# Kernel optimization log

Measured on AMD Instinct MI355X. Metric: run time of the kernel, lower is better.

Reference implementation:

```python
import jax, jax.numpy as jnp
import numpy as np

B, N, E = 4096, 64, 256      # graph pairs, nodes per drug, directed edges per drug
F, H, FP = 128, 64, 2048     # node feat dim, hidden dim, fingerprint dim


def setup_inputs() -> dict:
    key = jax.random.key(0)
    ks = jax.random.split(key, 14)
    return {
        "x1": jax.random.normal(ks[0], (B, N, F), jnp.float32),
        "x2": jax.random.normal(ks[1], (B, N, F), jnp.float32),
        "edge1": jax.random.randint(ks[2], (B, 2, E), 0, N, jnp.int32),
        "edge2": jax.random.randint(ks[3], (B, 2, E), 0, N, jnp.int32),
        "fp1": jax.random.uniform(ks[4], (B, FP), jnp.float32),
        "fp2": jax.random.uniform(ks[5], (B, FP), jnp.float32),
        "W1": jax.random.normal(ks[6], (F, H), jnp.float32) * 0.05,
        "b1": jnp.zeros((H,), jnp.float32),
        "W2": jax.random.normal(ks[7], (H, H), jnp.float32) * 0.05,
        "b2": jnp.zeros((H,), jnp.float32),
        "Wm1": jax.random.normal(ks[8], (2 * H + 2 * FP, 256), jnp.float32) * 0.02,
        "bm1": jnp.zeros((256,), jnp.float32),
        "Wm2": jax.random.normal(ks[9], (256, 1), jnp.float32) * 0.05,
        "bm2": jnp.zeros((1,), jnp.float32),
    }


def gcn_conv(x, src, dst, W, b):
    """PyG GCNConv: self-loops + symmetric normalization, aggregated at dst."""
    n = x.shape[0]
    loops = jnp.arange(n, dtype=src.dtype)
    s = jnp.concatenate([src, loops])
    d = jnp.concatenate([dst, loops])
    deg = jax.ops.segment_sum(jnp.ones_like(d, jnp.float32), d, num_segments=n)
    norm = jax.lax.rsqrt(deg)                      # deg >= 1 due to self-loops
    xw = x @ W                                     # [n, H]
    msg = xw[s] * (norm[s] * norm[d])[:, None]     # [n+E, H]
    return jax.ops.segment_sum(msg, d, num_segments=n) + b


def encode(x, edges, W1, b1, W2, b2):
    src, dst = edges[0], edges[1]
    h = jax.nn.relu(gcn_conv(x, src, dst, W1, b1))
    h = jax.nn.relu(gcn_conv(h, src, dst, W2, b2))
    return h.mean(axis=0)                          # global_mean_pool (1 graph)


_encode_b = jax.vmap(encode, in_axes=(0, 0, None, None, None, None))


def reference(x1, x2, edge1, edge2, fp1, fp2, W1, b1, W2, b2, Wm1, bm1, Wm2, bm2):
    h1 = _encode_b(x1, edge1, W1, b1, W2, b2)      # [B, H]
    h2 = _encode_b(x2, edge2, W1, b1, W2, b2)      # [B, H]
    fused = jnp.concatenate([h1, h2, fp1, fp2], axis=1)  # [B, 2H+2FP]
    hidden = jax.nn.relu(fused @ Wm1 + bm1)
    return jax.nn.sigmoid(hidden @ Wm2 + bm2).reshape(-1)
```

## Files before the change

kernel.cpp:

```cpp
#include <hip/hip_runtime.h>
#include <math.h>

#define B_PAIRS 4096
#define NNODES  64
#define NEDGES  256
#define FDIM    128
#define HDIM    64
#define FPDIM   2048
#define MDIM    256
#define KTOT    4224

typedef __attribute__((ext_vector_type(4))) float f32x4;
typedef __bf16 bf16x8 __attribute__((ext_vector_type(8)));

__device__ __forceinline__ unsigned short f2bf(float f) {
    return __builtin_bit_cast(unsigned short, (__bf16)f);
}
__device__ __forceinline__ unsigned pack2(float a, float b) {
    return (unsigned)f2bf(a) | ((unsigned)f2bf(b) << 16);
}
__device__ __forceinline__ unsigned long long pack4(float a, float b, float c, float d) {
    return (unsigned long long)pack2(a, b) | ((unsigned long long)pack2(c, d) << 32);
}

__global__ void prep_weights(const float* __restrict__ W1, const float* __restrict__ W2,
                             unsigned short* __restrict__ W1t, unsigned short* __restrict__ W2t) {
    const int t0 = blockIdx.x * 256 + threadIdx.x;
    const int stride = gridDim.x * 256;
    for (int i = t0; i < HDIM * FDIM; i += stride) {
        const int n = i >> 7, k = i & 127;
        W1t[i] = f2bf(W1[k * HDIM + n]);
    }
    for (int i = t0; i < HDIM * HDIM; i += stride) {
        const int n = i >> 6, k = i & 63;
        W2t[i] = f2bf(W2[k * HDIM + n]);
    }
}

__global__ __launch_bounds__(256)
void prep_wm1(const float* __restrict__ Wm1, unsigned short* __restrict__ Wm1t) {
    __shared__ float tile[32][33];
    const int k0 = blockIdx.x * 32, n0 = blockIdx.y * 32;
    const int t = threadIdx.x;
    const int c = t & 31, r8 = t >> 5;
    #pragma unroll
    for (int rr = r8; rr < 32; rr += 8)
        tile[rr][c] = Wm1[(size_t)(k0 + rr) * MDIM + n0 + c];
    __syncthreads();
    #pragma unroll
    for (int j = 0; j < 4; ++j) {
        const int n = n0 + r8 + 8 * j;
        Wm1t[(size_t)n * KTOT + k0 + c] = f2bf(tile[c][r8 + 8 * j]);
    }
}

#define WAITLDS() do { __asm__ volatile("s_waitcnt lgkmcnt(0)" ::: "memory"); \
                       __builtin_amdgcn_sched_barrier(0); } while (0)

__global__ __launch_bounds__(64, 2)
void encode_kernel(const float* __restrict__ x1, const float* __restrict__ x2,
                   const int* __restrict__ e1, const int* __restrict__ e2,
                   const unsigned short* __restrict__ W1t, const float* __restrict__ b1,
                   const unsigned short* __restrict__ W2t, const float* __restrict__ b2,
                   float* __restrict__ hbuf) {
    __shared__ __align__(16) unsigned char lds[24576];
    const int gid  = blockIdx.x;
    const int drug = gid >> 12;
    const int b    = gid & (B_PAIRS - 1);
    const float* x  = (drug ? x2 : x1) + (size_t)b * NNODES * FDIM;
    const int*   eg = (drug ? e2 : e1) + (size_t)b * 2 * NEDGES;

    const int t  = threadIdx.x;
    const int lr = t & 15, lg = t >> 4;
    const unsigned swl = (unsigned)(lr & 7) << 4;

    unsigned* cnt = (unsigned*)(lds + 8192);
    int*      deg = (int*)(lds + 16640);
    float*    nrm = (float*)(lds + 16896);

    float4 xa[32];
    #pragma unroll
    for (int mt = 0; mt < 4; ++mt) {
        const float* xr = x + (size_t)(16 * mt + lr) * FDIM + 8 * lg;
        #pragma unroll
        for (int ks = 0; ks < 4; ++ks) {
            xa[mt * 8 + 2 * ks]     = ((const float4*)(xr + 32 * ks))[0];
            xa[mt * 8 + 2 * ks + 1] = ((const float4*)(xr + 32 * ks))[1];
        }
    }
    const int4 s4 = ((const int4*)eg)[t];
    const int4 d4 = ((const int4*)eg)[t + 64];

    #pragma unroll
    for (int i = 0; i < 8; ++i) ((uint4*)cnt)[t + 64 * i] = make_uint4(0, 0, 0, 0);
    if (t < 16) ((uint4*)cnt)[512 + t] = make_uint4(0, 0, 0, 0);
    deg[t] = 0;
    WAITLDS();

    {
        const int ss[4] = {s4.x, s4.y, s4.z, s4.w};
        const int dd[4] = {d4.x, d4.y, d4.z, d4.w};
        #pragma unroll
        for (int i = 0; i < 4; ++i) {
            atomicAdd(&deg[dd[i]], 1);
            atomicAdd(&cnt[dd[i] * 33 + (ss[i] >> 1)], 1u << ((ss[i] & 1) * 16));
        }
    }
    WAITLDS();
    nrm[t] = rsqrtf((float)deg[t] + 1.0f);
    WAITLDS();

    bf16x8 bw1[16];
    #pragma unroll
    for (int nt = 0; nt < 4; ++nt)
        #pragma unroll
        for (int ks = 0; ks < 4; ++ks)
            bw1[nt * 4 + ks] = *(const bf16x8*)(W1t + (16 * nt + lr) * FDIM + 32 * ks + 8 * lg);

    {
        const int r = t;
        const float nr = nrm[r];
        unsigned char* arow = lds + r * 128;
        const unsigned sw = (unsigned)(r & 7) << 4;
        #pragma unroll
        for (int cw = 0; cw < 16; ++cw) {
            const unsigned w0 = cnt[r * 33 + 2 * cw];
            const unsigned w1 = cnt[r * 33 + 2 * cw + 1];
            const float4 nv = ((const float4*)nrm)[cw];
            const int c = 4 * cw;
            const float u0 = (float)((w0 & 0xffffu) + (r == c     ? 1u : 0u)) * nr * nv.x;
            const float u1 = (float)((w0 >> 16)     + (r == c + 1 ? 1u : 0u)) * nr * nv.y;
            const float u2 = (float)((w1 & 0xffffu) + (r == c + 2 ? 1u : 0u)) * nr * nv.z;
            const float u3 = (float)((w1 >> 16)     + (r == c + 3 ? 1u : 0u)) * nr * nv.w;
            *(unsigned long long*)(arow + (((unsigned)(8 * cw)) ^ sw)) = pack4(u0, u1, u2, u3);
        }
    }
    WAITLDS();

    #pragma unroll
    for (int mt = 0; mt < 4; ++mt) {
        f32x4 acc[4];
        #pragma unroll
        for (int nt = 0; nt < 4; ++nt) acc[nt] = (f32x4){0.f, 0.f, 0.f, 0.f};
        #pragma unroll
        for (int ks = 0; ks < 4; ++ks) {
            bf16x8 a;
            const float4 u = xa[mt * 8 + 2 * ks], v = xa[mt * 8 + 2 * ks + 1];
            a[0] = (__bf16)u.x; a[1] = (__bf16)u.y; a[2] = (__bf16)u.z; a[3] = (__bf16)u.w;
            a[4] = (__bf16)v.x; a[5] = (__bf16)v.y; a[6] = (__bf16)v.z; a[7] = (__bf16)v.w;
            #pragma unroll
            for (int nt = 0; nt < 4; ++nt)
                acc[nt] = __builtin_amdgcn_mfma_f32_16x16x32_bf16(a, bw1[nt * 4 + ks], acc[nt], 0, 0, 0);
        }
        const unsigned m2 = (unsigned)(2 * (16 * mt + 4 * lg));
        #pragma unroll
        for (int nt = 0; nt < 4; ++nt) {
            const int f = 16 * nt + lr;
            *(unsigned long long*)(lds + 8192u + (unsigned)f * 128 + (m2 ^ swl)) =
                pack4(acc[nt][0], acc[nt][1], acc[nt][2], acc[nt][3]);
        }
    }
    WAITLDS();

    {
        bf16x8 ba[8];
        #pragma unroll
        for (int nt = 0; nt < 4; ++nt)
            #pragma unroll
            for (int ks = 0; ks < 2; ++ks)
                ba[nt * 2 + ks] = *(const bf16x8*)(lds + (unsigned)(16 * nt + lr) * 128 +
                                                   (((unsigned)(64 * ks + 16 * lg)) ^ swl));
        #pragma unroll
        for (int mt = 0; mt < 4; ++mt) {
            f32x4 acc[4];
            #pragma unroll
            for (int nt = 0; nt < 4; ++nt) acc[nt] = (f32x4){0.f, 0.f, 0.f, 0.f};
            #pragma unroll
            for (int ks = 0; ks < 2; ++ks) {
                const bf16x8 a = *(const bf16x8*)(lds + 8192u + (unsigned)(16 * mt + lr) * 128 +
                                                  (((unsigned)(64 * ks + 16 * lg)) ^ swl));
                #pragma unroll
                for (int nt = 0; nt < 4; ++nt)
                    acc[nt] = __builtin_amdgcn_mfma_f32_16x16x32_bf16(a, ba[nt * 2 + ks], acc[nt], 0, 0, 0);
            }
            const int m0 = 16 * mt + 4 * lg;
            const float4 b1v = *(const float4*)(b1 + m0);
            const unsigned m2 = (unsigned)(2 * m0);
            #pragma unroll
            for (int nt = 0; nt < 4; ++nt) {
                const int d = 16 * nt + lr;
                const float v0 = fmaxf(acc[nt][0] + b1v.x, 0.f);
                const float v1 = fmaxf(acc[nt][1] + b1v.y, 0.f);
                const float v2 = fmaxf(acc[nt][2] + b1v.z, 0.f);
                const float v3 = fmaxf(acc[nt][3] + b1v.w, 0.f);
                *(unsigned long long*)(lds + 16384u + (unsigned)d * 128 + (m2 ^ swl)) =
                    pack4(v0, v1, v2, v3);
            }
        }
    }
    WAITLDS();

    {
        bf16x8 bw2[8];
        #pragma unroll
        for (int nt = 0; nt < 4; ++nt)
            #pragma unroll
            for (int ks = 0; ks < 2; ++ks)
                bw2[nt * 2 + ks] = *(const bf16x8*)(W2t + (16 * nt + lr) * HDIM + 32 * ks + 8 * lg);
        #pragma unroll
        for (int mt = 0; mt < 4; ++mt) {
            f32x4 acc[4];
            #pragma unroll
            for (int nt = 0; nt < 4; ++nt) acc[nt] = (f32x4){0.f, 0.f, 0.f, 0.f};
            #pragma unroll
            for (int ks = 0; ks < 2; ++ks) {
                const bf16x8 a = *(const bf16x8*)(lds + 16384u + (unsigned)(16 * mt + lr) * 128 +
                                                  (((unsigned)(64 * ks + 16 * lg)) ^ swl));
                #pragma unroll
                for (int nt = 0; nt < 4; ++nt)
                    acc[nt] = __builtin_amdgcn_mfma_f32_16x16x32_bf16(a, bw2[nt * 2 + ks], acc[nt], 0, 0, 0);
            }
            const unsigned m2 = (unsigned)(2 * (16 * mt + 4 * lg));
            #pragma unroll
            for (int nt = 0; nt < 4; ++nt) {
                const int n = 16 * nt + lr;
                *(unsigned long long*)(lds + 8192u + (unsigned)n * 128 + (m2 ^ swl)) =
                    pack4(acc[nt][0], acc[nt][1], acc[nt][2], acc[nt][3]);
            }
        }
    }
    WAITLDS();

    {
        bf16x8 bt3[8];
        #pragma unroll
        for (int nt = 0; nt < 4; ++nt)
            #pragma unroll
            for (int ks = 0; ks < 2; ++ks)
                bt3[nt * 2 + ks] = *(const bf16x8*)(lds + 8192u + (unsigned)(16 * nt + lr) * 128 +
                                                    (((unsigned)(64 * ks + 16 * lg)) ^ swl));
        float b2v[4], p[4];
        #pragma unroll
        for (int nt = 0; nt < 4; ++nt) { b2v[nt] = b2[16 * nt + lr]; p[nt] = 0.f; }
        #pragma unroll
        for (int mt = 0; mt < 4; ++mt) {
            f32x4 acc[4];
            #pragma unroll
            for (int nt = 0; nt < 4; ++nt) acc[nt] = (f32x4){0.f, 0.f, 0.f, 0.f};
            #pragma unroll
            for (int ks = 0; ks < 2; ++ks) {
                const bf16x8 a = *(const bf16x8*)(lds + (unsigned)(16 * mt + lr) * 128 +
                                                  (((unsigned)(64 * ks + 16 * lg)) ^ swl));
                #pragma unroll
                for (int nt = 0; nt < 4; ++nt)
                    acc[nt] = __builtin_amdgcn_mfma_f32_16x16x32_bf16(a, bt3[nt * 2 + ks], acc[nt], 0, 0, 0);
            }
            #pragma unroll
            for (int nt = 0; nt < 4; ++nt) {
                #pragma unroll
                for (int j = 0; j < 4; ++j) p[nt] += fmaxf(acc[nt][j] + b2v[nt], 0.f);
            }
        }
        #pragma unroll
        for (int nt = 0; nt < 4; ++nt) {
            p[nt] += __shfl_xor(p[nt], 16, 64);
            p[nt] += __shfl_xor(p[nt], 32, 64);
        }
        if (lg == 0) {
            float* hout = hbuf + ((size_t)drug * B_PAIRS + b) * HDIM;
            #pragma unroll
            for (int nt = 0; nt < 4; ++nt) hout[16 * nt + lr] = p[nt] * (1.0f / 64.0f);
        }
    }
}

__global__ __launch_bounds__(256)
void fused_mlp_kernel(const float* __restrict__ fp1, const float* __restrict__ fp2,
                      const float* __restrict__ hbuf,
                      const unsigned short* __restrict__ Wm1t,
                      const float* __restrict__ bm1, const float* __restrict__ Wm2,
                      const float* __restrict__ bm2, float* __restrict__ out) {
    __shared__ __align__(16) unsigned char lds[8448];
    float* pool = (float*)(lds + 8192);
    const int t = threadIdx.x;
    const int lane = t & 63, wid = t >> 6;
    const int lr = lane & 15, lg = lane >> 4;
    const int pair0 = blockIdx.x * 16;

    const int r  = t >> 4;
    const int kc = (t & 15) << 3;
    const int pr = pair0 + r;
    const unsigned wOff = (unsigned)r * 256 + (((unsigned)(2 * kc)) ^ ((unsigned)(r & 7) << 4));

    f32x4 acc[4];
    #pragma unroll
    for (int nf = 0; nf < 4; ++nf) acc[nf] = (f32x4){0.f, 0.f, 0.f, 0.f};

    const unsigned short* brow[4];
    #pragma unroll
    for (int nf = 0; nf < 4; ++nf)
        brow[nf] = Wm1t + (size_t)(64 * wid + 16 * nf + lr) * KTOT + 8 * lg;

    float4 va, vb;
    #define LOAD_A(s)                                                                  \
        {                                                                              \
            const float* src;                                                          \
            if ((s) == 0)                                                              \
                src = (kc < 64) ? hbuf + (size_t)pr * HDIM + kc                        \
                                : hbuf + (size_t)(B_PAIRS + pr) * HDIM + (kc - 64);    \
            else if ((s) <= 16)                                                        \
                src = fp1 + (size_t)pr * FPDIM + ((s) - 1) * 128 + kc;                 \
            else                                                                       \
                src = fp2 + (size_t)pr * FPDIM + ((s) - 17) * 128 + kc;                \
            va = ((const float4*)src)[0];                                              \
            vb = ((const float4*)src)[1];                                              \
        }
    #define STORE_A(base)                                                              \
        *(uint4*)((base) + wOff) = make_uint4(pack2(va.x, va.y), pack2(va.z, va.w),    \
                                              pack2(vb.x, vb.y), pack2(vb.z, vb.w));

    LOAD_A(0);
    STORE_A(lds);
    for (int s = 0; s < 33; ++s) {
        const bool more = (s + 1 < 33);
        if (more) LOAD_A(s + 1);
        __syncthreads();
        const unsigned char* buf = lds + (unsigned)((s & 1) << 12);
        const unsigned asw = (unsigned)(lr & 7) << 4;
        const int kglob = s << 7;
        #pragma unroll
        for (int ks = 0; ks < 4; ++ks) {
            const unsigned kb = (unsigned)(64 * ks + 16 * lg);
            const bf16x8 a = *(const bf16x8*)(buf + (unsigned)lr * 256 + (kb ^ asw));
            #pragma unroll
            for (int nf = 0; nf < 4; ++nf) {
                const bf16x8 bw = *(const bf16x8*)(brow[nf] + kglob + 32 * ks);
                acc[nf] = __builtin_amdgcn_mfma_f32_16x16x32_bf16(a, bw, acc[nf], 0, 0, 0);
            }
        }
        if (more) STORE_A(lds + (unsigned)(((s + 1) & 1) << 12));
    }

    float bm1v[4], wm2v[4];
    #pragma unroll
    for (int nf = 0; nf < 4; ++nf) {
        const int n = 64 * wid + 16 * nf + lr;
        bm1v[nf] = bm1[n];
        wm2v[nf] = Wm2[n];
    }
    #pragma unroll
    for (int reg = 0; reg < 4; ++reg) {
        float p = 0.f;
        #pragma unroll
        for (int nf = 0; nf < 4; ++nf)
            p += fmaxf(acc[nf][reg] + bm1v[nf], 0.f) * wm2v[nf];
        p += __shfl_xor(p, 1, 64);
        p += __shfl_xor(p, 2, 64);
        p += __shfl_xor(p, 4, 64);
        p += __shfl_xor(p, 8, 64);
        if (lr == 0) pool[wid * 16 + 4 * lg + reg] = p;
    }
    __syncthreads();
    if (t < 16) {
        const float y = pool[t] + pool[16 + t] + pool[32 + t] + pool[48 + t] + bm2[0];
        out[pair0 + t] = 1.0f / (1.0f + expf(-y));
    }
    #undef LOAD_A
    #undef STORE_A
}

extern "C" void kernel_launch(void* const* d_in, const int* in_sizes, int n_in,
                              void* d_out, int out_size, void* d_ws, size_t ws_size,
                              hipStream_t stream) {
    const float* x1  = (const float*)d_in[0];
    const float* x2  = (const float*)d_in[1];
    const int*   e1  = (const int*)d_in[2];
    const int*   e2  = (const int*)d_in[3];
    const float* fp1 = (const float*)d_in[4];
    const float* fp2 = (const float*)d_in[5];
    const float* W1  = (const float*)d_in[6];
    const float* b1  = (const float*)d_in[7];
    const float* W2  = (const float*)d_in[8];
    const float* b2  = (const float*)d_in[9];
    const float* Wm1 = (const float*)d_in[10];
    const float* bm1 = (const float*)d_in[11];
    const float* Wm2 = (const float*)d_in[12];
    const float* bm2 = (const float*)d_in[13];
    float* out  = (float*)d_out;

    float* hbuf = (float*)d_ws;
    unsigned short* W1t  = (unsigned short*)((char*)d_ws + (2 << 20));
    unsigned short* W2t  = W1t + HDIM * FDIM;
    unsigned short* Wm1t = (unsigned short*)((char*)d_ws + (3 << 20));

    hipLaunchKernelGGL(prep_weights, dim3(16), dim3(256), 0, stream, W1, W2, W1t, W2t);
    hipLaunchKernelGGL(prep_wm1, dim3(132, 8), dim3(256), 0, stream, Wm1, Wm1t);
    hipLaunchKernelGGL(encode_kernel, dim3(2 * B_PAIRS), dim3(64), 0, stream,
                       x1, x2, e1, e2, W1t, b1, W2t, b2, hbuf);
    hipLaunchKernelGGL(fused_mlp_kernel, dim3(B_PAIRS / 16), dim3(256), 0, stream,
                       fp1, fp2, hbuf, Wm1t, bm1, Wm2, bm2, out);
}
```

Measured before the change: 170.1 us.

## Shrink encoder LDS footprint by reusing buffers and splitting feature loads

Cuts the encoder's shared-memory allocation by loading each stage's A tile into registers before overwriting the same LDS region in place. The buffer at offset 16384 goes away and the norm/degree arrays are repacked. The x feature prefetch is split into two halves, with the second half loaded after the edge-count phase, which lowers peak register pressure. The aim is to fit more workgroups per CU for better latency hiding, at the cost of extra waits and a later second load of x.

```diff
diff --git a/kernel.cpp b/kernel.cpp
--- a/kernel.cpp
+++ b/kernel.cpp
@@ -63,7 +63,7 @@
                    const unsigned short* __restrict__ W1t, const float* __restrict__ b1,
                    const unsigned short* __restrict__ W2t, const float* __restrict__ b2,
                    float* __restrict__ hbuf) {
-    __shared__ __align__(16) unsigned char lds[24576];
+    __shared__ __align__(16) unsigned char lds[17152];
     const int gid  = blockIdx.x;
     const int drug = gid >> 12;
     const int b    = gid & (B_PAIRS - 1);
@@ -75,17 +75,17 @@
     const unsigned swl = (unsigned)(lr & 7) << 4;
 
     unsigned* cnt = (unsigned*)(lds + 8192);
-    int*      deg = (int*)(lds + 16640);
-    float*    nrm = (float*)(lds + 16896);
-
-    float4 xa[32];
-    #pragma unroll
-    for (int mt = 0; mt < 4; ++mt) {
+    float*    nrm = (float*)(lds + 16640);
+    int*      deg = (int*)(lds + 16896);
+
+    float4 xalo[16];
+    #pragma unroll
+    for (int mt = 0; mt < 2; ++mt) {
         const float* xr = x + (size_t)(16 * mt + lr) * FDIM + 8 * lg;
         #pragma unroll
         for (int ks = 0; ks < 4; ++ks) {
-            xa[mt * 8 + 2 * ks]     = ((const float4*)(xr + 32 * ks))[0];
-            xa[mt * 8 + 2 * ks + 1] = ((const float4*)(xr + 32 * ks))[1];
+            xalo[mt * 8 + 2 * ks]     = ((const float4*)(xr + 32 * ks))[0];
+            xalo[mt * 8 + 2 * ks + 1] = ((const float4*)(xr + 32 * ks))[1];
         }
     }
     const int4 s4 = ((const int4*)eg)[t];
@@ -107,6 +107,18 @@
         }
     }
     WAITLDS();
+
+    float4 xahi[16];
+    #pragma unroll
+    for (int mt = 0; mt < 2; ++mt) {
+        const float* xr = x + (size_t)(16 * (mt + 2) + lr) * FDIM + 8 * lg;
+        #pragma unroll
+        for (int ks = 0; ks < 4; ++ks) {
+            xahi[mt * 8 + 2 * ks]     = ((const float4*)(xr + 32 * ks))[0];
+            xahi[mt * 8 + 2 * ks + 1] = ((const float4*)(xr + 32 * ks))[1];
+        }
+    }
+
     nrm[t] = rsqrtf((float)deg[t] + 1.0f);
     WAITLDS();
 
@@ -138,38 +150,50 @@
     WAITLDS();
 
     #pragma unroll
-    for (int mt = 0; mt < 4; ++mt) {
-        f32x4 acc[4];
-        #pragma unroll
-        for (int nt = 0; nt < 4; ++nt) acc[nt] = (f32x4){0.f, 0.f, 0.f, 0.f};
-        #pragma unroll
-        for (int ks = 0; ks < 4; ++ks) {
-            bf16x8 a;
-            const float4 u = xa[mt * 8 + 2 * ks], v = xa[mt * 8 + 2 * ks + 1];
-            a[0] = (__bf16)u.x; a[1] = (__bf16)u.y; a[2] = (__bf16)u.z; a[3] = (__bf16)u.w;
-            a[4] = (__bf16)v.x; a[5] = (__bf16)v.y; a[6] = (__bf16)v.z; a[7] = (__bf16)v.w;
-            #pragma unroll
-            for (int nt = 0; nt < 4; ++nt)
-                acc[nt] = __builtin_amdgcn_mfma_f32_16x16x32_bf16(a, bw1[nt * 4 + ks], acc[nt], 0, 0, 0);
-        }
-        const unsigned m2 = (unsigned)(2 * (16 * mt + 4 * lg));
-        #pragma unroll
-        for (int nt = 0; nt < 4; ++nt) {
-            const int f = 16 * nt + lr;
-            *(unsigned long long*)(lds + 8192u + (unsigned)f * 128 + (m2 ^ swl)) =
-                pack4(acc[nt][0], acc[nt][1], acc[nt][2], acc[nt][3]);
+    for (int half = 0; half < 2; ++half) {
+        const float4* xs = half ? xahi : xalo;
+        #pragma unroll
+        for (int m2i = 0; m2i < 2; ++m2i) {
+            const int mt = half * 2 + m2i;
+            f32x4 acc[4];
+            #pragma unroll
+            for (int nt = 0; nt < 4; ++nt) acc[nt] = (f32x4){0.f, 0.f, 0.f, 0.f};
+            #pragma unroll
+            for (int ks = 0; ks < 4; ++ks) {
+                bf16x8 a;
+                const float4 u = xs[m2i * 8 + 2 * ks], v = xs[m2i * 8 + 2 * ks + 1];
+                a[0] = (__bf16)u.x; a[1] = (__bf16)u.y; a[2] = (__bf16)u.z; a[3] = (__bf16)u.w;
+                a[4] = (__bf16)v.x; a[5] = (__bf16)v.y; a[6] = (__bf16)v.z; a[7] = (__bf16)v.w;
+                #pragma unroll
+                for (int nt = 0; nt < 4; ++nt)
+                    acc[nt] = __builtin_amdgcn_mfma_f32_16x16x32_bf16(a, bw1[nt * 4 + ks], acc[nt], 0, 0, 0);
+            }
+            const unsigned m2 = (unsigned)(2 * (16 * mt + 4 * lg));
+            #pragma unroll
+            for (int nt = 0; nt < 4; ++nt) {
+                const int f = 16 * nt + lr;
+                *(unsigned long long*)(lds + 8192u + (unsigned)f * 128 + (m2 ^ swl)) =
+                    pack4(acc[nt][0], acc[nt][1], acc[nt][2], acc[nt][3]);
+            }
         }
     }
     WAITLDS();
 
     {
-        bf16x8 ba[8];
+        bf16x8 ta[8], ba[8];
+        #pragma unroll
+        for (int mt = 0; mt < 4; ++mt)
+            #pragma unroll
+            for (int ks = 0; ks < 2; ++ks)
+                ta[mt * 2 + ks] = *(const bf16x8*)(lds + 8192u + (unsigned)(16 * mt + lr) * 128 +
+                                                   (((unsigned)(64 * ks + 16 * lg)) ^ swl));
         #pragma unroll
         for (int nt = 0; nt < 4; ++nt)
             #pragma unroll
             for (int ks = 0; ks < 2; ++ks)
                 ba[nt * 2 + ks] = *(const bf16x8*)(lds + (unsigned)(16 * nt + lr) * 128 +
                                                    (((unsigned)(64 * ks + 16 * lg)) ^ swl));
+        WAITLDS();
         #pragma unroll
         for (int mt = 0; mt < 4; ++mt) {
             f32x4 acc[4];
@@ -177,11 +201,9 @@
             for (int nt = 0; nt < 4; ++nt) acc[nt] = (f32x4){0.f, 0.f, 0.f, 0.f};
             #pragma unroll
             for (int ks = 0; ks < 2; ++ks) {
-                const bf16x8 a = *(const bf16x8*)(lds + 8192u + (unsigned)(16 * mt + lr) * 128 +
-                                                  (((unsigned)(64 * ks + 16 * lg)) ^ swl));
                 #pragma unroll
                 for (int nt = 0; nt < 4; ++nt)
-                    acc[nt] = __builtin_amdgcn_mfma_f32_16x16x32_bf16(a, ba[nt * 2 + ks], acc[nt], 0, 0, 0);
+                    acc[nt] = __builtin_amdgcn_mfma_f32_16x16x32_bf16(ta[mt * 2 + ks], ba[nt * 2 + ks], acc[nt], 0, 0, 0);
             }
             const int m0 = 16 * mt + 4 * lg;
             const float4 b1v = *(const float4*)(b1 + m0);
@@ -193,7 +215,7 @@
                 const float v1 = fmaxf(acc[nt][1] + b1v.y, 0.f);
                 const float v2 = fmaxf(acc[nt][2] + b1v.z, 0.f);
                 const float v3 = fmaxf(acc[nt][3] + b1v.w, 0.f);
-                *(unsigned long long*)(lds + 16384u + (unsigned)d * 128 + (m2 ^ swl)) =
+                *(unsigned long long*)(lds + 8192u + (unsigned)d * 128 + (m2 ^ swl)) =
                     pack4(v0, v1, v2, v3);
             }
         }
@@ -201,12 +223,19 @@
     WAITLDS();
 
     {
-        bf16x8 bw2[8];
+        bf16x8 ta[8], bw2[8];
+        #pragma unroll
+        for (int mt = 0; mt < 4; ++mt)
+            #pragma unroll
+            for (int ks = 0; ks < 2; ++ks)
+                ta[mt * 2 + ks] = *(const bf16x8*)(lds + 8192u + (unsigned)(16 * mt + lr) * 128 +
+                                                   (((unsigned)(64 * ks + 16 * lg)) ^ swl));
         #pragma unroll
         for (int nt = 0; nt < 4; ++nt)
             #pragma unroll
             for (int ks = 0; ks < 2; ++ks)
                 bw2[nt * 2 + ks] = *(const bf16x8*)(W2t + (16 * nt + lr) * HDIM + 32 * ks + 8 * lg);
+        WAITLDS();
         #pragma unroll
         for (int mt = 0; mt < 4; ++mt) {
             f32x4 acc[4];
@@ -214,11 +243,9 @@
             for (int nt = 0; nt < 4; ++nt) acc[nt] = (f32x4){0.f, 0.f, 0.f, 0.f};
             #pragma unroll
             for (int ks = 0; ks < 2; ++ks) {
-                const bf16x8 a = *(const bf16x8*)(lds + 16384u + (unsigned)(16 * mt + lr) * 128 +
-                                                  (((unsigned)(64 * ks + 16 * lg)) ^ swl));
                 #pragma unroll
                 for (int nt = 0; nt < 4; ++nt)
-                    acc[nt] = __builtin_amdgcn_mfma_f32_16x16x32_bf16(a, bw2[nt * 2 + ks], acc[nt], 0, 0, 0);
+                    acc[nt] = __builtin_amdgcn_mfma_f32_16x16x32_bf16(ta[mt * 2 + ks], bw2[nt * 2 + ks], acc[nt], 0, 0, 0);
             }
             const unsigned m2 = (unsigned)(2 * (16 * mt + 4 * lg));
             #pragma unroll
```

After: 162.3 us. -4.6%, faster.
